# Kernel optimization log

Hardware: AMD Instinct MI355X
Metric: run time of the kernel (lower is better)

Reference implementation:

```python
import jax, jax.numpy as jnp
import numpy as np

B, T, C = 4, 2048, 1024
NH = 16
HD = C // NH
ROPE_BASE = 10000.0


def setup_inputs() -> dict:
    key = jax.random.key(0)
    k1, k2, k3, k4, k5 = jax.random.split(key, 5)
    s = 1.0 / np.sqrt(C)
    return {
        "x": jax.random.normal(k1, (B, T, C), dtype=jnp.float32),
        "W_qkv": jax.random.normal(k2, (C, 3 * C), dtype=jnp.float32) * s,
        "b_qkv": jax.random.normal(k3, (3 * C,), dtype=jnp.float32) * 0.02,
        "W_proj": jax.random.normal(k4, (C, C), dtype=jnp.float32) * s,
        "b_proj": jax.random.normal(k5, (C,), dtype=jnp.float32) * 0.02,
    }


def _rotate_half(u):
    u1, u2 = u[..., : HD // 2], u[..., HD // 2 :]
    return jnp.concatenate((-u2, u1), axis=-1)


def _rope_cos_sin(t, dtype):
    # inv_freq: [HD/2]; positions: [T]
    inv_freq = 1.0 / (ROPE_BASE ** (jnp.arange(0, HD, 2, dtype=jnp.float32) / HD))
    pos = jnp.arange(t, dtype=jnp.float32)
    freqs = pos[:, None] * inv_freq[None, :]          # [T, HD/2]
    emb = jnp.concatenate((freqs, freqs), axis=-1)    # [T, HD]
    return jnp.cos(emb).astype(dtype), jnp.sin(emb).astype(dtype)


def reference(x, W_qkv, b_qkv, W_proj, b_proj):
    b, t, c = x.shape
    qkv = x @ W_qkv + b_qkv                           # [B,T,3C]
    q, k, v = jnp.split(qkv, 3, axis=-1)
    # [B,T,C] -> [B,NH,T,HD]
    def to_heads(u):
        return u.reshape(b, t, NH, HD).transpose(0, 2, 1, 3)
    q, k, v = to_heads(q), to_heads(k), to_heads(v)
    cos, sin = _rope_cos_sin(t, x.dtype)              # [T,HD] each; broadcast over B,NH
    q = q * cos + _rotate_half(q) * sin
    k = k * cos + _rotate_half(k) * sin
    att = jnp.einsum("bhqd,bhkd->bhqk", q, k) * (1.0 / np.sqrt(HD))
    causal = jnp.tril(jnp.ones((t, t), dtype=bool))
    att = jnp.where(causal, att, -jnp.inf)
    att = jax.nn.softmax(att, axis=-1)
    y = jnp.einsum("bhqk,bhkd->bhqd", att, v)         # [B,NH,T,HD]
    y = y.transpose(0, 2, 1, 3).reshape(b, t, c)
    return y @ W_proj + b_proj
```

## Files before the change

kernel.cpp:

```cpp
#include <hip/hip_runtime.h>
#include <cstdint>
#include <cstddef>

typedef __attribute__((ext_vector_type(8))) short short8;
typedef __attribute__((ext_vector_type(4))) float float4x;
typedef __attribute__((ext_vector_type(16))) float float16x;
typedef __attribute__((ext_vector_type(2))) unsigned int uint2v;

__device__ __forceinline__ uint16_t f2b(float f){
  uint32_t u = __builtin_bit_cast(uint32_t, f);
  u += 0x7FFFu + ((u >> 16) & 1u);
  return (uint16_t)(u >> 16);
}
__device__ __forceinline__ float b2f(uint16_t h){
  uint32_t u = ((uint32_t)h) << 16;
  return __builtin_bit_cast(float, u);
}
__device__ __forceinline__ float4x zero4(){
  float4x v; v[0]=0.f; v[1]=0.f; v[2]=0.f; v[3]=0.f; return v;
}
__device__ __forceinline__ float16x zero16(){
  float16x v;
#pragma unroll
  for (int i = 0; i < 16; i++) v[i] = 0.f;
  return v;
}
__device__ __forceinline__ uint32_t cvtpk(float lo, float hi){
  uint32_t r;
  asm("v_cvt_pk_bf16_f32 %0, %1, %2" : "=v"(r) : "v"(lo), "v"(hi));
  return r;
}
__device__ __forceinline__ void plswap(uint32_t &a, uint32_t &b){
#if __has_builtin(__builtin_amdgcn_permlane32_swap)
  uint2v r = __builtin_amdgcn_permlane32_swap(a, b, false, false);
  a = r[0]; b = r[1];
#else
  uint32_t a2 = (uint32_t)__shfl_xor((int)a, 32, 64);
  uint32_t b2 = (uint32_t)__shfl_xor((int)b, 32, 64);
  bool lo = ((threadIdx.x & 63) < 32);
  uint32_t an = lo ? a : b2;
  uint32_t bn = lo ? a2 : b;
  a = an; b = bn;
#endif
}
__device__ __forceinline__ float fexp2(float x){
#if __has_builtin(__builtin_amdgcn_exp2f)
  return __builtin_amdgcn_exp2f(x);
#else
  return exp2f(x);
#endif
}
__device__ __forceinline__ void gload16(const uint16_t* g, uint16_t* l){
  __builtin_amdgcn_global_load_lds(
      (const __attribute__((address_space(1))) uint32_t*)g,
      (__attribute__((address_space(3))) uint32_t*)l, 16, 0, 0);
}

__global__ __launch_bounds__(256) void k_f32_to_bf16(const float* __restrict__ in,
                                                     uint16_t* __restrict__ out, int n4){
  int i = blockIdx.x * 256 + threadIdx.x;
  if (i < n4){
    float4 v = ((const float4*)in)[i];
    ushort4 o;
    o.x = f2b(v.x); o.y = f2b(v.y); o.z = f2b(v.z); o.w = f2b(v.w);
    ((ushort4*)out)[i] = o;
  }
}

__global__ __launch_bounds__(256) void k_transpose_bf16(const float* __restrict__ W,
                                                        uint16_t* __restrict__ Wt, int K, int N){
  __shared__ float tile[32][33];
  int k0 = blockIdx.y * 32, n0 = blockIdx.x * 32;
  int c = threadIdx.x & 31, r0 = threadIdx.x >> 5;
  for (int rr = r0; rr < 32; rr += 8)
    tile[rr][c] = W[(size_t)(k0 + rr) * N + n0 + c];
  __syncthreads();
  for (int rr = r0; rr < 32; rr += 8)
    Wt[(size_t)(n0 + rr) * K + k0 + c] = f2b(tile[c][rr]);
}

template<int OUTF>
__global__ __launch_bounds__(256, 3) void k_gemm_bt(const uint16_t* __restrict__ A,
                                                    const uint16_t* __restrict__ Bt,
                                                    const float* __restrict__ bias,
                                                    void* __restrict__ Cout,
                                                    int M, int N, int K){
  __shared__ __align__(16) uint16_t As[2][128*32];
  __shared__ __align__(16) uint16_t Bs[2][128*32];
  const int tid = threadIdx.x, lane = tid & 63, wave = tid >> 6;
  const int wr = wave >> 1, wc = wave & 1;
  const int m0 = blockIdx.y * 128, n0 = blockIdx.x * 128;
  const int quad = lane >> 4, l15 = lane & 15;
  const int rowA = tid >> 2, chA = tid & 3;

  float4x acc[4][4];
  for (int i = 0; i < 4; i++) for (int j = 0; j < 4; j++) acc[i][j] = zero4();

  const uint16_t* pa0 = &A[(size_t)(m0 + rowA)*K + chA*8];
  const uint16_t* pa1 = &A[(size_t)(m0 + rowA + 64)*K + chA*8];
  const uint16_t* pb0 = &Bt[(size_t)(n0 + rowA)*K + chA*8];
  const uint16_t* pb1 = &Bt[(size_t)(n0 + rowA + 64)*K + chA*8];

  gload16(pa0, &As[0][tid*8]);
  gload16(pa1, &As[0][64*32 + tid*8]);
  gload16(pb0, &Bs[0][tid*8]);
  gload16(pb1, &Bs[0][64*32 + tid*8]);

  int buf = 0;
  for (int k0 = 0; k0 < K; k0 += 32){
    __syncthreads();
    if (k0 + 32 < K){
      int nb = buf ^ 1;
      gload16(pa0 + k0 + 32, &As[nb][tid*8]);
      gload16(pa1 + k0 + 32, &As[nb][64*32 + tid*8]);
      gload16(pb0 + k0 + 32, &Bs[nb][tid*8]);
      gload16(pb1 + k0 + 32, &Bs[nb][64*32 + tid*8]);
    }
    short8 af[4], bf[4];
#pragma unroll
    for (int mt = 0; mt < 4; mt++)
      af[mt] = *(const short8*)&As[buf][(wr*64 + mt*16 + l15)*32 + quad*8];
#pragma unroll
    for (int nt = 0; nt < 4; nt++)
      bf[nt] = *(const short8*)&Bs[buf][(wc*64 + nt*16 + l15)*32 + quad*8];
#pragma unroll
    for (int mt = 0; mt < 4; mt++)
#pragma unroll
      for (int nt = 0; nt < 4; nt++)
        acc[mt][nt] = __builtin_amdgcn_mfma_f32_16x16x32_bf16(af[mt], bf[nt], acc[mt][nt], 0, 0, 0);
    buf ^= 1;
  }

#pragma unroll
  for (int mt = 0; mt < 4; mt++){
    int grow = m0 + wr*64 + mt*16 + quad*4;
#pragma unroll
    for (int nt = 0; nt < 4; nt++){
      int gcol = n0 + wc*64 + nt*16 + l15;
      float bv = bias[gcol];
#pragma unroll
      for (int r = 0; r < 4; r++){
        float v = acc[mt][nt][r] + bv;
        if (OUTF) ((float*)Cout)[(size_t)(grow + r)*N + gcol] = v;
        else      ((uint16_t*)Cout)[(size_t)(grow + r)*N + gcol] = f2b(v);
      }
    }
  }
}

__global__ __launch_bounds__(256) void k_rope(uint16_t* __restrict__ qkv){
  int idx = blockIdx.x * 256 + threadIdx.x;
  int i = idx & 31;
  int h = (idx >> 5) & 15;
  int t = (idx >> 9) & 2047;
  int b = (idx >> 20) & 3;
  int which = idx >> 22;
  size_t base = ((size_t)(b*2048 + t))*3072 + (size_t)which*1024 + h*64 + i;
  float u1 = b2f(qkv[base]), u2 = b2f(qkv[base + 32]);
  float inv = exp2f(-(float)i * 0.4152410118609203f);
  float ang = (float)t * inv;
  float s, c;
  __sincosf(ang, &s, &c);
  qkv[base]      = f2b(u1*c - u2*s);
  qkv[base + 32] = f2b(u2*c + u1*s);
}

__global__ __launch_bounds__(256) void k_transpose_v(const uint16_t* __restrict__ qkv,
                                                     uint16_t* __restrict__ vt){
  __shared__ __align__(16) uint16_t tile[64*72];
  int bh = blockIdx.y;
  int t0 = blockIdx.x * 64;
  int b = bh >> 4, h = bh & 15;
  int r = threadIdx.x >> 2, ch = threadIdx.x & 3;
  const uint16_t* src = &qkv[((size_t)(b*2048 + t0 + r))*3072 + 2048 + h*64];
  *(uint4*)&tile[r*72 + ch*8]      = *(const uint4*)&src[ch*8];
  *(uint4*)&tile[r*72 + 32 + ch*8] = *(const uint4*)&src[32 + ch*8];
  __syncthreads();
  short8 v0, v1;
#pragma unroll
  for (int j = 0; j < 8; j++) v0[j] = (short)tile[(ch*8 + j)*72 + r];
#pragma unroll
  for (int j = 0; j < 8; j++) v1[j] = (short)tile[(32 + ch*8 + j)*72 + r];
  uint16_t* dst = &vt[((size_t)(bh*64 + r))*2048 + t0];
  *(short8*)&dst[ch*8]      = v0;
  *(short8*)&dst[32 + ch*8] = v1;
}

__global__ __launch_bounds__(256) void k_attn(const uint16_t* __restrict__ qkv,
                                              const uint16_t* __restrict__ vt,
                                              uint16_t* __restrict__ y){
  __shared__ __align__(16) uint16_t Klds[2][64*64];
  __shared__ __align__(16) uint16_t Vlds[2][64*64];

  const int Did = blockIdx.x;
  const int g = Did & 7, ii = Did >> 3;
  const int bh = g*8 + (ii >> 3);
  const int X  = ii & 7;
  const int b = bh >> 4, h = bh & 15;
  const int lane = threadIdx.x & 63, w = threadIdx.x >> 6;
  const int l31 = lane & 31, hi = lane >> 5;

  const uint16_t* Qbase  = qkv + (size_t)b*2048*3072 + h*64;
  const uint16_t* Kbase  = qkv + (size_t)b*2048*3072 + 1024 + h*64;
  const uint16_t* Vtbase = vt  + (size_t)bh*64*2048;

  const float S2 = 0.18033688011112042f;
  const float M2 = 43.28085122666890f;

  const int isV  = w >> 1;
  const int rbase = (w & 1) * 32;
  const int rsub = lane >> 3, csub = lane & 7;

  const int cA = X, cB = 15 - X;
  const int KT_A = 2*cA + 2;
  const int TS = 34;

  int c = cA;
  int qr = c*128 + w*32;

  short8 aq[4];
#pragma unroll
  for (int kc = 0; kc < 4; kc++)
    aq[kc] = *(const short8*)&Qbase[(size_t)(qr + l31)*3072 + kc*16 + hi*8];

  float16x o[2];
  o[0] = zero16(); o[1] = zero16();
  float lr4[4] = {0.f, 0.f, 0.f, 0.f};

  auto epilogue = [&](){
    float l = (lr4[0] + lr4[1]) + (lr4[2] + lr4[3]);
    l += __shfl_xor(l, 32, 64);
    float linv = 1.f / l;
    float lv[16];
#pragma unroll
    for (int r = 0; r < 16; r++)
      lv[r] = __shfl(linv, (r&3) + 8*(r>>2) + 4*hi, 64);
#pragma unroll
    for (int dt = 0; dt < 2; dt++)
#pragma unroll
      for (int r = 0; r < 16; r++){
        int row = (r&3) + 8*(r>>2) + 4*hi;
        y[((size_t)(b*2048 + qr + row))*1024 + h*64 + dt*32 + l31] = f2b(o[dt][r] * lv[r]);
      }
  };

#pragma unroll
  for (int j = 0; j < 4; j++){
    int r  = rbase + j*8 + rsub;
    int cg = csub ^ (r & 7);
    if (isV) gload16(Vtbase + (size_t)r*2048 + cg*8, &Vlds[0][(rbase + j*8)*64 + lane*8]);
    else     gload16(Kbase  + (size_t)r*3072 + cg*8, &Klds[0][(rbase + j*8)*64 + lane*8]);
  }

  int cur = 0;
  for (int t = 0; t < TS; ++t){
    __syncthreads();
    const int kt = (t < KT_A) ? t : t - KT_A;
    if (t + 1 < TS){
      const int ktn = (t + 1 < KT_A) ? t + 1 : t + 1 - KT_A;
      int nb = cur ^ 1;
#pragma unroll
      for (int j = 0; j < 4; j++){
        int r  = rbase + j*8 + rsub;
        int cg = csub ^ (r & 7);
        if (isV) gload16(Vtbase + (size_t)r*2048 + (size_t)ktn*64 + cg*8,
                         &Vlds[nb][(rbase + j*8)*64 + lane*8]);
        else     gload16(Kbase  + (size_t)(ktn*64 + r)*3072 + cg*8,
                         &Klds[nb][(rbase + j*8)*64 + lane*8]);
      }
    }

    if (t == KT_A){
      epilogue();
      c = cB; qr = c*128 + w*32;
#pragma unroll
      for (int kc = 0; kc < 4; kc++)
        aq[kc] = *(const short8*)&Qbase[(size_t)(qr + l31)*3072 + kc*16 + hi*8];
      o[0] = zero16(); o[1] = zero16();
      lr4[0] = lr4[1] = lr4[2] = lr4[3] = 0.f;
    }

    float16x p0 = zero16(), p1 = zero16();
    __builtin_amdgcn_s_setprio(1);
#pragma unroll
    for (int kc = 0; kc < 4; kc++){
      const int ch = 2*kc + hi;
      short8 ak0 = *(const short8*)&Klds[cur][(l31)*64      + ((ch ^ (l31 & 7))*8)];
      short8 ak1 = *(const short8*)&Klds[cur][(32 + l31)*64 + ((ch ^ (l31 & 7))*8)];
      p0 = __builtin_amdgcn_mfma_f32_32x32x16_bf16(ak0, aq[kc], p0, 0, 0, 0);
      p1 = __builtin_amdgcn_mfma_f32_32x32x16_bf16(ak1, aq[kc], p1, 0, 0, 0);
    }
    __builtin_amdgcn_s_setprio(0);

    if (kt >= 2*c){
      const int tq = qr + l31;
#pragma unroll
      for (int r = 0; r < 16; r++){
        int kb = kt*64 + (r&3) + 8*(r>>2) + 4*hi;
        if (kb > tq)      p0[r] = -1e30f;
        if (kb + 32 > tq) p1[r] = -1e30f;
      }
    }

#pragma unroll
    for (int r = 0; r < 16; r++){
      float e0 = fexp2(__builtin_fmaf(p0[r], S2, -M2));
      float e1 = fexp2(__builtin_fmaf(p1[r], S2, -M2));
      lr4[r & 3] += e0 + e1;
      p0[r] = e0; p1[r] = e1;
    }

    __builtin_amdgcn_s_setprio(1);
#pragma unroll
    for (int kc = 0; kc < 4; kc++){
      const int e8 = (kc & 1)*8;
      uint32_t w0, w1, w2, w3;
      if (kc < 2){
        w0 = cvtpk(p0[e8+0], p0[e8+1]); w1 = cvtpk(p0[e8+2], p0[e8+3]);
        w2 = cvtpk(p0[e8+4], p0[e8+5]); w3 = cvtpk(p0[e8+6], p0[e8+7]);
      } else {
        w0 = cvtpk(p1[e8+0], p1[e8+1]); w1 = cvtpk(p1[e8+2], p1[e8+3]);
        w2 = cvtpk(p1[e8+4], p1[e8+5]); w3 = cvtpk(p1[e8+6], p1[e8+7]);
      }
      plswap(w0, w2);
      plswap(w1, w3);
      union { uint32_t u[4]; short8 s; } ap;
      ap.u[0] = w0; ap.u[1] = w1; ap.u[2] = w2; ap.u[3] = w3;

      const int ch = 2*kc + hi;
      short8 bv0 = *(const short8*)&Vlds[cur][(l31)*64      + ((ch ^ (l31 & 7))*8)];
      short8 bv1 = *(const short8*)&Vlds[cur][(32 + l31)*64 + ((ch ^ (l31 & 7))*8)];
      o[0] = __builtin_amdgcn_mfma_f32_32x32x16_bf16(ap.s, bv0, o[0], 0, 0, 0);
      o[1] = __builtin_amdgcn_mfma_f32_32x32x16_bf16(ap.s, bv1, o[1], 0, 0, 0);
    }
    __builtin_amdgcn_s_setprio(0);
    cur ^= 1;
  }

  epilogue();
}

extern "C" void kernel_launch(void* const* d_in, const int* in_sizes, int n_in,
                              void* d_out, int out_size, void* d_ws, size_t ws_size,
                              hipStream_t stream){
  const float* x     = (const float*)d_in[0];
  const float* Wqkv  = (const float*)d_in[1];
  const float* bqkv  = (const float*)d_in[2];
  const float* Wproj = (const float*)d_in[3];
  const float* bproj = (const float*)d_in[4];

  uint16_t* p = (uint16_t*)d_ws;
  uint16_t* xb    = p; p += (size_t)8192*1024;
  uint16_t* wqkvt = p; p += (size_t)3072*1024;
  uint16_t* wprjt = p; p += (size_t)1024*1024;
  uint16_t* qkv   = p; p += (size_t)8192*3072;
  uint16_t* vt    = p; p += (size_t)64*64*2048;
  uint16_t* yb    = p; p += (size_t)8192*1024;

  k_f32_to_bf16<<<8192, 256, 0, stream>>>(x, xb, 2097152);
  k_transpose_bf16<<<dim3(96, 32), 256, 0, stream>>>(Wqkv, wqkvt, 1024, 3072);
  k_transpose_bf16<<<dim3(32, 32), 256, 0, stream>>>(Wproj, wprjt, 1024, 1024);
  k_gemm_bt<0><<<dim3(24, 64), 256, 0, stream>>>(xb, wqkvt, bqkv, (void*)qkv, 8192, 3072, 1024);
  k_rope<<<32768, 256, 0, stream>>>(qkv);
  k_transpose_v<<<dim3(32, 64), 256, 0, stream>>>(qkv, vt);
  k_attn<<<512, 256, 0, stream>>>(qkv, vt, yb);
  k_gemm_bt<1><<<dim3(8, 64), 256, 0, stream>>>(yb, wprjt, bproj, d_out, 8192, 1024, 1024);
}
```

Before: 283.2 us.

## Fuse RoPE and V transpose into the QKV GEMM epilogue

The QKV GEMM epilogue now applies RoPE directly to the Q and K tiles. It pairs accumulator columns nt and nt+2 so that the elements 32 apart share a thread, and computes sin/cos in registers. V tiles are staged through shared memory and written straight into the transposed vt layout. This removes two standalone kernels and their full read/write passes over the qkv buffer. The cost is extra transcendental work and an LDS staging step in the epilogue, which adds some register and shared-memory pressure.

```diff
diff --git a/kernel.cpp b/kernel.cpp
--- a/kernel.cpp
+++ b/kernel.cpp
@@ -79,12 +79,116 @@
     Wt[(size_t)(n0 + rr) * K + k0 + c] = f2b(tile[c][rr]);
 }
 
-template<int OUTF>
-__global__ __launch_bounds__(256, 3) void k_gemm_bt(const uint16_t* __restrict__ A,
-                                                    const uint16_t* __restrict__ Bt,
-                                                    const float* __restrict__ bias,
-                                                    void* __restrict__ Cout,
-                                                    int M, int N, int K){
+__global__ __launch_bounds__(256, 3) void k_gemm_qkv(const uint16_t* __restrict__ A,
+                                                     const uint16_t* __restrict__ Bt,
+                                                     const float* __restrict__ bias,
+                                                     uint16_t* __restrict__ qkv,
+                                                     uint16_t* __restrict__ vt){
+  const int K = 1024;
+  __shared__ __align__(16) uint16_t SM[18432];
+  uint16_t* As_ = SM;
+  uint16_t* Bs_ = SM + 8192;
+  const int tid = threadIdx.x, lane = tid & 63, wave = tid >> 6;
+  const int wr = wave >> 1, wc = wave & 1;
+  const int m0 = blockIdx.y * 128, n0 = blockIdx.x * 128;
+  const int quad = lane >> 4, l15 = lane & 15;
+  const int rowA = tid >> 2, chA = tid & 3;
+
+  float4x acc[4][4];
+  for (int i = 0; i < 4; i++) for (int j = 0; j < 4; j++) acc[i][j] = zero4();
+
+  const uint16_t* pa0 = &A[(size_t)(m0 + rowA)*K + chA*8];
+  const uint16_t* pa1 = &A[(size_t)(m0 + rowA + 64)*K + chA*8];
+  const uint16_t* pb0 = &Bt[(size_t)(n0 + rowA)*K + chA*8];
+  const uint16_t* pb1 = &Bt[(size_t)(n0 + rowA + 64)*K + chA*8];
+
+  gload16(pa0, &As_[tid*8]);
+  gload16(pa1, &As_[64*32 + tid*8]);
+  gload16(pb0, &Bs_[tid*8]);
+  gload16(pb1, &Bs_[64*32 + tid*8]);
+
+  int buf = 0;
+  for (int k0 = 0; k0 < K; k0 += 32){
+    __syncthreads();
+    if (k0 + 32 < K){
+      int nb = buf ^ 1;
+      gload16(pa0 + k0 + 32, &As_[nb*4096 + tid*8]);
+      gload16(pa1 + k0 + 32, &As_[nb*4096 + 64*32 + tid*8]);
+      gload16(pb0 + k0 + 32, &Bs_[nb*4096 + tid*8]);
+      gload16(pb1 + k0 + 32, &Bs_[nb*4096 + 64*32 + tid*8]);
+    }
+    short8 af[4], bfr[4];
+#pragma unroll
+    for (int mt = 0; mt < 4; mt++)
+      af[mt] = *(const short8*)&As_[buf*4096 + (wr*64 + mt*16 + l15)*32 + quad*8];
+#pragma unroll
+    for (int nt = 0; nt < 4; nt++)
+      bfr[nt] = *(const short8*)&Bs_[buf*4096 + (wc*64 + nt*16 + l15)*32 + quad*8];
+#pragma unroll
+    for (int mt = 0; mt < 4; mt++)
+#pragma unroll
+      for (int nt = 0; nt < 4; nt++)
+        acc[mt][nt] = __builtin_amdgcn_mfma_f32_16x16x32_bf16(af[mt], bfr[nt], acc[mt][nt], 0, 0, 0);
+    buf ^= 1;
+  }
+
+  if (blockIdx.x < 16){
+#pragma unroll
+    for (int mt = 0; mt < 4; mt++){
+      int grow = m0 + wr*64 + mt*16 + quad*4;
+      int tpos = grow & 2047;
+#pragma unroll
+      for (int nt = 0; nt < 2; nt++){
+        int gcol = n0 + wc*64 + nt*16 + l15;
+        float bv1 = bias[gcol], bv2 = bias[gcol + 32];
+        int i = nt*16 + l15;
+        float inv = exp2f(-(float)i * 0.4152410118609203f);
+#pragma unroll
+        for (int r = 0; r < 4; r++){
+          float ang = (float)(tpos + r) * inv;
+          float s, c;
+          __sincosf(ang, &s, &c);
+          float u1 = acc[mt][nt][r]   + bv1;
+          float u2 = acc[mt][nt+2][r] + bv2;
+          qkv[(size_t)(grow + r)*3072 + gcol]      = f2b(u1*c - u2*s);
+          qkv[(size_t)(grow + r)*3072 + gcol + 32] = f2b(u2*c + u1*s);
+        }
+      }
+    }
+  } else {
+    __syncthreads();
+    uint16_t* T = &SM[wave*4608];
+#pragma unroll
+    for (int mt = 0; mt < 4; mt++)
+#pragma unroll
+      for (int nt = 0; nt < 4; nt++){
+        int gcol = n0 + wc*64 + nt*16 + l15;
+        float bv = bias[gcol];
+#pragma unroll
+        for (int r = 0; r < 4; r++)
+          T[(nt*16 + l15)*72 + mt*16 + quad*4 + r] = f2b(acc[mt][nt][r] + bv);
+      }
+    __syncthreads();
+    const int h = (n0 + wc*64 - 2048) >> 6;
+    const int tg0 = m0 + wr*64;
+    const int bb = tg0 >> 11, tb = tg0 & 2047;
+    const int bh64 = (bb*16 + h)*64;
+    const int d32 = lane & 31, th = lane >> 5;
+#pragma unroll
+    for (int dd = 0; dd < 2; dd++)
+#pragma unroll
+      for (int it = 0; it < 4; it++){
+        short8 v = *(const short8*)&T[(d32 + 32*dd)*72 + th*32 + it*8];
+        *(short8*)&vt[((size_t)(bh64 + d32 + 32*dd))*2048 + tb + th*32 + it*8] = v;
+      }
+  }
+}
+
+__global__ __launch_bounds__(256, 3) void k_gemm_proj(const uint16_t* __restrict__ A,
+                                                      const uint16_t* __restrict__ Bt,
+                                                      const float* __restrict__ bias,
+                                                      float* __restrict__ Cout,
+                                                      int M, int N, int K){
   __shared__ __align__(16) uint16_t As[2][128*32];
   __shared__ __align__(16) uint16_t Bs[2][128*32];
   const int tid = threadIdx.x, lane = tid & 63, wave = tid >> 6;
@@ -116,18 +220,18 @@
       gload16(pb0 + k0 + 32, &Bs[nb][tid*8]);
       gload16(pb1 + k0 + 32, &Bs[nb][64*32 + tid*8]);
     }
-    short8 af[4], bf[4];
+    short8 af[4], bfr[4];
 #pragma unroll
     for (int mt = 0; mt < 4; mt++)
       af[mt] = *(const short8*)&As[buf][(wr*64 + mt*16 + l15)*32 + quad*8];
 #pragma unroll
     for (int nt = 0; nt < 4; nt++)
-      bf[nt] = *(const short8*)&Bs[buf][(wc*64 + nt*16 + l15)*32 + quad*8];
+      bfr[nt] = *(const short8*)&Bs[buf][(wc*64 + nt*16 + l15)*32 + quad*8];
 #pragma unroll
     for (int mt = 0; mt < 4; mt++)
 #pragma unroll
       for (int nt = 0; nt < 4; nt++)
-        acc[mt][nt] = __builtin_amdgcn_mfma_f32_16x16x32_bf16(af[mt], bf[nt], acc[mt][nt], 0, 0, 0);
+        acc[mt][nt] = __builtin_amdgcn_mfma_f32_16x16x32_bf16(af[mt], bfr[nt], acc[mt][nt], 0, 0, 0);
     buf ^= 1;
   }
 
@@ -139,51 +243,10 @@
       int gcol = n0 + wc*64 + nt*16 + l15;
       float bv = bias[gcol];
 #pragma unroll
-      for (int r = 0; r < 4; r++){
-        float v = acc[mt][nt][r] + bv;
-        if (OUTF) ((float*)Cout)[(size_t)(grow + r)*N + gcol] = v;
-        else      ((uint16_t*)Cout)[(size_t)(grow + r)*N + gcol] = f2b(v);
-      }
-    }
-  }
-}
-
-__global__ __launch_bounds__(256) void k_rope(uint16_t* __restrict__ qkv){
-  int idx = blockIdx.x * 256 + threadIdx.x;
-  int i = idx & 31;
-  int h = (idx >> 5) & 15;
-  int t = (idx >> 9) & 2047;
-  int b = (idx >> 20) & 3;
-  int which = idx >> 22;
-  size_t base = ((size_t)(b*2048 + t))*3072 + (size_t)which*1024 + h*64 + i;
-  float u1 = b2f(qkv[base]), u2 = b2f(qkv[base + 32]);
-  float inv = exp2f(-(float)i * 0.4152410118609203f);
-  float ang = (float)t * inv;
-  float s, c;
-  __sincosf(ang, &s, &c);
-  qkv[base]      = f2b(u1*c - u2*s);
-  qkv[base + 32] = f2b(u2*c + u1*s);
-}
-
-__global__ __launch_bounds__(256) void k_transpose_v(const uint16_t* __restrict__ qkv,
-                                                     uint16_t* __restrict__ vt){
-  __shared__ __align__(16) uint16_t tile[64*72];
-  int bh = blockIdx.y;
-  int t0 = blockIdx.x * 64;
-  int b = bh >> 4, h = bh & 15;
-  int r = threadIdx.x >> 2, ch = threadIdx.x & 3;
-  const uint16_t* src = &qkv[((size_t)(b*2048 + t0 + r))*3072 + 2048 + h*64];
-  *(uint4*)&tile[r*72 + ch*8]      = *(const uint4*)&src[ch*8];
-  *(uint4*)&tile[r*72 + 32 + ch*8] = *(const uint4*)&src[32 + ch*8];
-  __syncthreads();
-  short8 v0, v1;
-#pragma unroll
-  for (int j = 0; j < 8; j++) v0[j] = (short)tile[(ch*8 + j)*72 + r];
-#pragma unroll
-  for (int j = 0; j < 8; j++) v1[j] = (short)tile[(32 + ch*8 + j)*72 + r];
-  uint16_t* dst = &vt[((size_t)(bh*64 + r))*2048 + t0];
-  *(short8*)&dst[ch*8]      = v0;
-  *(short8*)&dst[32 + ch*8] = v1;
+      for (int r = 0; r < 4; r++)
+        Cout[(size_t)(grow + r)*N + gcol] = acc[mt][nt][r] + bv;
+    }
+  }
 }
 
 __global__ __launch_bounds__(256) void k_attn(const uint16_t* __restrict__ qkv,
@@ -360,9 +423,7 @@
   k_f32_to_bf16<<<8192, 256, 0, stream>>>(x, xb, 2097152);
   k_transpose_bf16<<<dim3(96, 32), 256, 0, stream>>>(Wqkv, wqkvt, 1024, 3072);
   k_transpose_bf16<<<dim3(32, 32), 256, 0, stream>>>(Wproj, wprjt, 1024, 1024);
-  k_gemm_bt<0><<<dim3(24, 64), 256, 0, stream>>>(xb, wqkvt, bqkv, (void*)qkv, 8192, 3072, 1024);
-  k_rope<<<32768, 256, 0, stream>>>(qkv);
-  k_transpose_v<<<dim3(32, 64), 256, 0, stream>>>(qkv, vt);
+  k_gemm_qkv<<<dim3(24, 64), 256, 0, stream>>>(xb, wqkvt, bqkv, qkv, vt);
   k_attn<<<512, 256, 0, stream>>>(qkv, vt, yb);
-  k_gemm_bt<1><<<dim3(8, 64), 256, 0, stream>>>(yb, wprjt, bproj, d_out, 8192, 1024, 1024);
-}
+  k_gemm_proj<<<dim3(8, 64), 256, 0, stream>>>(yb, wprjt, bproj, (float*)d_out, 8192, 1024, 1024);
+}
```

Measured after the change: 261.5 us. 1.08x faster.
